# Optimization experiments

Measured on AMD Instinct MI355X. Metric: run time of the kernel, lower is better.

The kernel has to match this reference:

```python
import jax, jax.numpy as jnp
import numpy as np

N_NODES = 100000
N_EDGES = 1600000
D = 128


def setup_inputs() -> dict:
    key = jax.random.key(0)
    k1, k2, k3, k4 = jax.random.split(key, 4)
    ego_embeddings = jax.random.normal(k1, (N_NODES, D), dtype=jnp.float32)
    edge_index = jax.random.randint(k2, (2, N_EDGES), 0, N_NODES, dtype=jnp.int64)
    edge_weight = jax.random.uniform(k3, (N_EDGES,), dtype=jnp.float32)
    W = jax.random.normal(k4, (D, D), dtype=jnp.float32) * (1.0 / np.sqrt(D))
    b = jnp.zeros((D,), dtype=jnp.float32)
    return {"ego_embeddings": ego_embeddings, "edge_index": edge_index,
            "edge_weight": edge_weight, "W": W, "b": b}


def reference(ego_embeddings, edge_index, edge_weight, W, b):
    # SpMM: side[i] = sum_j A[i,j] * ego[j], A given as COO (dst=row, src=col)
    src = edge_index[1]
    dst = edge_index[0]
    messages = ego_embeddings[src] * edge_weight[:, None]  # [E, D]
    side_embeddings = jax.ops.segment_sum(messages, dst, num_segments=N_NODES)
    # gcn aggregator: LeakyReLU(Linear(ego + side)); dropout p=0.0 -> identity
    h = (ego_embeddings + side_embeddings) @ W.T + b
    return jax.nn.leaky_relu(h, negative_slope=0.01)
```

## Files before the change

### kernel.cpp

```cpp
#include <hip/hip_runtime.h>

#define N_NODES 100000
#define N_EDGES 1600000
#define DIM 128
#define CAP 48

#define NBIN 1563
#define BINW 64
#define BCAP 1280
#define EPT  8
#define EPB  2048

#define WB_OFF   0
#define GCUR_OFF 32768
#define DEG_OFF  65536
#define EPK_OFF  465536
#define EGOB_OFF (EPK_OFF + (size_t)N_NODES * CAP * 4)
#define WS_BF16  (EGOB_OFF + (size_t)N_NODES * DIM * 2)

using short8  = __attribute__((ext_vector_type(8))) short;
using floatx4 = __attribute__((ext_vector_type(4))) float;

static __device__ __forceinline__ unsigned short f2bf(float f) {
    unsigned u = __float_as_uint(f);
    u += 0x7FFF + ((u >> 16) & 1);
    return (unsigned short)(u >> 16);
}
static __device__ __forceinline__ float bf_lo(unsigned u) {
    return __uint_as_float(u << 16);
}
static __device__ __forceinline__ float bf_hi(unsigned u) {
    return __uint_as_float(u & 0xFFFF0000u);
}

#define EGO_BLKS 6250
__global__ __launch_bounds__(256) void convert_all(
        const float4* __restrict__ e4, uint4* __restrict__ o4,
        const float* __restrict__ W, unsigned short* __restrict__ Wb,
        int* __restrict__ gcur) {
    const int b = blockIdx.x;
    const int tid = threadIdx.x;
    if (b < EGO_BLKS) {
        int i = b * 256 + tid;
        float4 a = e4[2 * i];
        float4 c = e4[2 * i + 1];
        uint4 o;
        o.x = (unsigned)f2bf(a.x) | ((unsigned)f2bf(a.y) << 16);
        o.y = (unsigned)f2bf(a.z) | ((unsigned)f2bf(a.w) << 16);
        o.z = (unsigned)f2bf(c.x) | ((unsigned)f2bf(c.y) << 16);
        o.w = (unsigned)f2bf(c.z) | ((unsigned)f2bf(c.w) << 16);
        o4[i] = o;
    } else {
        int j = (b - EGO_BLKS) * 256 + tid;
        if (j < DIM * DIM) Wb[j] = f2bf(W[j]);
        if (j < NBIN) gcur[j] = 0;
    }
}

__global__ __launch_bounds__(256) void convert_w(const float* __restrict__ W,
                                                 unsigned short* __restrict__ Wb) {
    int i = blockIdx.x * 256 + threadIdx.x;
    if (i < DIM * DIM) Wb[i] = f2bf(W[i]);
}

__global__ __launch_bounds__(256) void bin_edges(
        const int* __restrict__ eidx,
        const float* __restrict__ ew,
        int* __restrict__ gcur,
        uint2* __restrict__ stg) {
    __shared__ int lh[NBIN];
    __shared__ int gb[NBIN];
    const int tid = threadIdx.x;
    const int b0 = blockIdx.x * EPB;

    for (int i = tid; i < NBIN; i += 256) lh[i] = 0;
    __syncthreads();

    int dst[EPT], rank[EPT];
    unsigned rec[EPT];
    bool val[EPT];
#pragma unroll
    for (int k = 0; k < EPT; ++k) {
        int e = b0 + k * 256 + tid;
        val[k] = e < N_EDGES;
        int ec = val[k] ? e : 0;
        int d = eidx[ec];
        int s = eidx[N_EDGES + ec];
        float w = ew[ec];
        dst[k] = d;
        rec[k] = ((unsigned)s << 15) | (unsigned)(w * 32767.0f + 0.5f);
        rank[k] = val[k] ? atomicAdd(&lh[d >> 6], 1) : 0;
    }
    __syncthreads();

    for (int i = tid; i < NBIN; i += 256) {
        int c = lh[i];
        gb[i] = c ? atomicAdd(&gcur[i], c) : 0;
    }
    __syncthreads();

#pragma unroll
    for (int k = 0; k < EPT; ++k) {
        if (val[k]) {
            int bin = dst[k] >> 6;
            int pos = gb[bin] + rank[k];
            if (pos < BCAP)
                stg[(size_t)bin * BCAP + pos] = make_uint2(rec[k], (unsigned)dst[k]);
        }
    }
}

__global__ __launch_bounds__(256) void place_edges(
        const uint2* __restrict__ stg,
        const int* __restrict__ gcur,
        unsigned* __restrict__ epk,
        int* __restrict__ deg) {
    __shared__ int lc[BINW];
    const int tid = threadIdx.x;
    const int bin = blockIdx.x;

    if (tid < BINW) lc[tid] = 0;
    __syncthreads();

    int cnt = gcur[bin];
    if (cnt > BCAP) cnt = BCAP;
    for (int r = tid; r < cnt; r += 256) {
        uint2 rc = stg[(size_t)bin * BCAP + r];
        int d = (int)rc.y;
        int rk = atomicAdd(&lc[d & (BINW - 1)], 1);
        if (rk < CAP) epk[(size_t)d * CAP + rk] = rc.x;
    }
    __syncthreads();

    if (tid < BINW) {
        int node = bin * BINW + tid;
        if (node < N_NODES) deg[node] = lc[tid];
    }
}

__global__ __launch_bounds__(256) void csr_scatter(
        const int* __restrict__ eidx,
        const float* __restrict__ ew,
        int* __restrict__ deg,
        unsigned* __restrict__ epk) {
    int e = blockIdx.x * 256 + threadIdx.x;
    if (e >= N_EDGES) return;
    int dst = eidx[e];
    int src = eidx[N_EDGES + e];
    float w = ew[e];
    int r = atomicAdd(&deg[dst], 1);
    if (r < CAP) {
        unsigned q = (unsigned)(w * 32767.0f + 0.5f);
        epk[(size_t)dst * CAP + r] = ((unsigned)src << 15) | q;
    }
}

#define LSTR 136
template <bool BF16>
__global__ __launch_bounds__(256, 6) void gather_gemm(
        const unsigned* __restrict__ eg2,
        const float* __restrict__ egof,
        const unsigned* __restrict__ epk,
        const int* __restrict__ deg,
        const unsigned short* __restrict__ Wb,
        const float* __restrict__ bias,
        float* __restrict__ out) {
    __shared__ __align__(16) unsigned short s_x[64 * LSTR];

    const int tid  = threadIdx.x;
    const int wave = tid >> 6;
    const int lane = tid & 63;
    const int R    = blockIdx.x * 64;
    const float inv15 = 1.0f / 32767.0f;

    if (BF16) {
        const int half = lane >> 5;
        const int hl   = lane & 31;
        const uint2* eg8 = (const uint2*)eg2;
        const int plane = (lane < CAP) ? lane : (CAP - 1);

        int nA = R + wave * 16;
        int nB = nA + 1;
        unsigned pvA = (nA < N_NODES) ? epk[(size_t)nA * CAP + plane] : 0u;
        unsigned pvB = (nB < N_NODES) ? epk[(size_t)nB * CAP + plane] : 0u;
        int dgA = (nA < N_NODES) ? deg[nA] : 0;
        int dgB = (nB < N_NODES) ? deg[nB] : 0;

        for (int i = 0; i < 8; ++i) {
            const int myNode = R + wave * 16 + 2 * i + half;
            const bool valid = myNode < N_NODES;

            unsigned pvAc = pvA, pvBc = pvB;
            int dgAc = dgA < CAP ? dgA : CAP;
            int dgBc = dgB < CAP ? dgB : CAP;
            const int dgme = half ? dgBc : dgAc;
            const int dgw  = dgAc > dgBc ? dgAc : dgBc;

            if (i < 7) {
                int mA = R + wave * 16 + 2 * (i + 1);
                int mB = mA + 1;
                pvA = (mA < N_NODES) ? epk[(size_t)mA * CAP + plane] : 0u;
                pvB = (mB < N_NODES) ? epk[(size_t)mB * CAP + plane] : 0u;
                dgA = (mA < N_NODES) ? deg[mA] : 0;
                dgB = (mB < N_NODES) ? deg[mB] : 0;
            }

            uint2 idv = make_uint2(0u, 0u);
            if (valid) idv = eg8[(size_t)myNode * 32 + hl];

            float acc[4][4];
#pragma unroll
            for (int k = 0; k < 4; ++k)
#pragma unroll
                for (int c = 0; c < 4; ++c) acc[k][c] = 0.f;
            acc[0][0] = bf_lo(idv.x);  acc[0][1] = bf_hi(idv.x);
            acc[0][2] = bf_lo(idv.y);  acc[0][3] = bf_hi(idv.y);

            for (int e = 0; e < dgw; e += 8) {
                unsigned p[8];
                uint2 g[8];
#pragma unroll
                for (int k = 0; k < 8; ++k) {
                    unsigned pa = __shfl(pvAc, e + k);
                    unsigned pb = __shfl(pvBc, e + k);
                    unsigned ps = half ? pb : pa;
                    p[k] = ((e + k) < dgme) ? ps : 0u;
                }
#pragma unroll
                for (int k = 0; k < 8; ++k)
                    g[k] = eg8[(size_t)(p[k] >> 15) * 32 + hl];
#pragma unroll
                for (int k = 0; k < 8; ++k) {
                    float wv = (float)(p[k] & 0x7FFF) * inv15;
                    acc[k & 3][0] = fmaf(wv, bf_lo(g[k].x), acc[k & 3][0]);
                    acc[k & 3][1] = fmaf(wv, bf_hi(g[k].x), acc[k & 3][1]);
                    acc[k & 3][2] = fmaf(wv, bf_lo(g[k].y), acc[k & 3][2]);
                    acc[k & 3][3] = fmaf(wv, bf_hi(g[k].y), acc[k & 3][3]);
                }
            }

            float s0 = (acc[0][0] + acc[1][0]) + (acc[2][0] + acc[3][0]);
            float s1 = (acc[0][1] + acc[1][1]) + (acc[2][1] + acc[3][1]);
            float s2 = (acc[0][2] + acc[1][2]) + (acc[2][2] + acc[3][2]);
            float s3 = (acc[0][3] + acc[1][3]) + (acc[2][3] + acc[3][3]);

            unsigned lo = (unsigned)f2bf(s0) | ((unsigned)f2bf(s1) << 16);
            unsigned hi = (unsigned)f2bf(s2) | ((unsigned)f2bf(s3) << 16);
            int myRow = wave * 16 + 2 * i + half;
            *(uint2*)&s_x[myRow * LSTR + hl * 4] = make_uint2(lo, hi);
        }
    } else {
        for (int i = 0; i < 16; ++i) {
            int node = R + wave * 16 + i;
            float ax = 0.f, ay = 0.f, bx = 0.f, by = 0.f;
            float cx = 0.f, cy = 0.f, dx2 = 0.f, dy2 = 0.f;
            if (node < N_NODES) {
                size_t cidx = (size_t)node * 64 + lane;
                float2 vv = ((const float2*)egof)[cidx];
                ax = vv.x; ay = vv.y;
                int dg = deg[node];
                if (dg > CAP) dg = CAP;
                size_t base = (size_t)node * CAP;
                unsigned pv = epk[base + (lane < CAP ? lane : CAP - 1)];
                int e = 0;
                for (; e + 3 < dg; e += 4) {
                    unsigned p0 = __shfl(pv, e + 0);
                    unsigned p1 = __shfl(pv, e + 1);
                    unsigned p2 = __shfl(pv, e + 2);
                    unsigned p3 = __shfl(pv, e + 3);
                    float2 v0 = ((const float2*)egof)[(size_t)(p0 >> 15) * 64 + lane];
                    float2 v1 = ((const float2*)egof)[(size_t)(p1 >> 15) * 64 + lane];
                    float2 v2 = ((const float2*)egof)[(size_t)(p2 >> 15) * 64 + lane];
                    float2 v3 = ((const float2*)egof)[(size_t)(p3 >> 15) * 64 + lane];
                    float w0 = (float)(p0 & 0x7FFF) * inv15;
                    float w1 = (float)(p1 & 0x7FFF) * inv15;
                    float w2 = (float)(p2 & 0x7FFF) * inv15;
                    float w3 = (float)(p3 & 0x7FFF) * inv15;
                    ax = fmaf(w0, v0.x, ax);  ay = fmaf(w0, v0.y, ay);
                    bx = fmaf(w1, v1.x, bx);  by = fmaf(w1, v1.y, by);
                    cx = fmaf(w2, v2.x, cx);  cy = fmaf(w2, v2.y, cy);
                    dx2 = fmaf(w3, v3.x, dx2); dy2 = fmaf(w3, v3.y, dy2);
                }
                for (; e < dg; ++e) {
                    unsigned p = __shfl(pv, e);
                    float2 vv2 = ((const float2*)egof)[(size_t)(p >> 15) * 64 + lane];
                    float w = (float)(p & 0x7FFF) * inv15;
                    ax = fmaf(w, vv2.x, ax);  ay = fmaf(w, vv2.y, ay);
                }
            }
            unsigned pk = (unsigned)f2bf(ax + bx + cx + dx2) |
                          ((unsigned)f2bf(ay + by + cy + dy2) << 16);
            *(unsigned*)&s_x[(wave * 16 + i) * LSTR + 2 * lane] = pk;
        }
    }

    const int m0 = wave * 16;
    const int ml = lane & 15;
    const int q  = lane >> 4;

    floatx4 acc[8];
#pragma unroll
    for (int nt = 0; nt < 8; ++nt) acc[nt] = (floatx4){0.f, 0.f, 0.f, 0.f};

#pragma unroll
    for (int kc = 0; kc < 4; ++kc) {
        short8 a = *(const short8*)&s_x[(m0 + ml) * LSTR + kc * 32 + q * 8];
#pragma unroll
        for (int nt = 0; nt < 8; ++nt) {
            short8 b = *(const short8*)&Wb[(size_t)(nt * 16 + ml) * DIM + kc * 32 + q * 8];
            acc[nt] = __builtin_amdgcn_mfma_f32_16x16x32_bf16(a, b, acc[nt], 0, 0, 0);
        }
    }

#pragma unroll
    for (int nt = 0; nt < 8; ++nt) {
        int col = nt * 16 + ml;
        float bv = bias[col];
#pragma unroll
        for (int r = 0; r < 4; ++r) {
            int row = R + m0 + q * 4 + r;
            if (row < N_NODES) {
                float v = acc[nt][r] + bv;
                v = v > 0.f ? v : 0.01f * v;
                out[(size_t)row * DIM + col] = v;
            }
        }
    }
}

extern "C" void kernel_launch(void* const* d_in, const int* in_sizes, int n_in,
                              void* d_out, int out_size, void* d_ws, size_t ws_size,
                              hipStream_t stream) {
    const float* ego  = (const float*)d_in[0];
    const int*   eidx = (const int*)d_in[1];
    const float* ew   = (const float*)d_in[2];
    const float* W    = (const float*)d_in[3];
    const float* bias = (const float*)d_in[4];
    float* out = (float*)d_out;

    char* ws = (char*)d_ws;
    unsigned short* Wb   = (unsigned short*)(ws + WB_OFF);
    int*            gcur = (int*)(ws + GCUR_OFF);
    int*            deg  = (int*)(ws + DEG_OFF);
    unsigned*       epk  = (unsigned*)(ws + EPK_OFF);
    unsigned short* egob = (unsigned short*)(ws + EGOB_OFF);
    uint2*          stg  = (uint2*)out;

    const bool use_bf16 = (ws_size >= WS_BF16);

    if (use_bf16) {
        convert_all<<<EGO_BLKS + 64, 256, 0, stream>>>(
            (const float4*)ego, (uint4*)egob, W, Wb, gcur);
        bin_edges<<<(N_EDGES + EPB - 1) / EPB, 256, 0, stream>>>(
            eidx, ew, gcur, stg);
        place_edges<<<NBIN, 256, 0, stream>>>(stg, gcur, epk, deg);
        gather_gemm<true><<<(N_NODES + 63) / 64, 256, 0, stream>>>(
            (const unsigned*)egob, ego, epk, deg, Wb, bias, out);
    } else {
        convert_w<<<(DIM * DIM + 255) / 256, 256, 0, stream>>>(W, Wb);
        hipMemsetAsync(deg, 0, (size_t)N_NODES * sizeof(int), stream);
        csr_scatter<<<(N_EDGES + 255) / 256, 256, 0, stream>>>(
            eidx, ew, deg, epk);
        gather_gemm<false><<<(N_NODES + 63) / 64, 256, 0, stream>>>(
            (const unsigned*)egob, ego, epk, deg, Wb, bias, out);
    }
}
```

Baseline: 265.8 us.

## Replace binned edge placement with direct atomic scatter and shrink gather blocks

Drops the two-pass bin_edges/place_edges build of the padded per-node edge lists. It goes back to a single csr_scatter kernel that does a global atomicAdd per edge on the degree array, which convert_all now zeroes. The gather_gemm kernel moves from 64-row, 256-thread blocks to 32-row, 128-thread blocks, doubling the block count for better occupancy and tail balance. The risk is that contended global atomics and scattered epk writes cost more than the binned path they replace, and smaller blocks reuse each W tile across fewer rows.

Result: slower. 314.1 us (+18.1%).

```diff
diff --git a/kernel.cpp b/kernel.cpp
--- a/kernel.cpp
+++ b/kernel.cpp
@@ -5,14 +5,7 @@
 #define DIM 128
 #define CAP 48
 
-#define NBIN 1563
-#define BINW 64
-#define BCAP 1280
-#define EPT  8
-#define EPB  2048
-
 #define WB_OFF   0
-#define GCUR_OFF 32768
 #define DEG_OFF  65536
 #define EPK_OFF  465536
 #define EGOB_OFF (EPK_OFF + (size_t)N_NODES * CAP * 4)
@@ -34,10 +27,11 @@
 }
 
 #define EGO_BLKS 6250
+#define TAIL_BLKS 391
 __global__ __launch_bounds__(256) void convert_all(
         const float4* __restrict__ e4, uint4* __restrict__ o4,
         const float* __restrict__ W, unsigned short* __restrict__ Wb,
-        int* __restrict__ gcur) {
+        int* __restrict__ deg) {
     const int b = blockIdx.x;
     const int tid = threadIdx.x;
     if (b < EGO_BLKS) {
@@ -53,7 +47,7 @@
     } else {
         int j = (b - EGO_BLKS) * 256 + tid;
         if (j < DIM * DIM) Wb[j] = f2bf(W[j]);
-        if (j < NBIN) gcur[j] = 0;
+        if (j < N_NODES) deg[j] = 0;
     }
 }
 
@@ -61,81 +55,6 @@
                                                  unsigned short* __restrict__ Wb) {
     int i = blockIdx.x * 256 + threadIdx.x;
     if (i < DIM * DIM) Wb[i] = f2bf(W[i]);
-}
-
-__global__ __launch_bounds__(256) void bin_edges(
-        const int* __restrict__ eidx,
-        const float* __restrict__ ew,
-        int* __restrict__ gcur,
-        uint2* __restrict__ stg) {
-    __shared__ int lh[NBIN];
-    __shared__ int gb[NBIN];
-    const int tid = threadIdx.x;
-    const int b0 = blockIdx.x * EPB;
-
-    for (int i = tid; i < NBIN; i += 256) lh[i] = 0;
-    __syncthreads();
-
-    int dst[EPT], rank[EPT];
-    unsigned rec[EPT];
-    bool val[EPT];
-#pragma unroll
-    for (int k = 0; k < EPT; ++k) {
-        int e = b0 + k * 256 + tid;
-        val[k] = e < N_EDGES;
-        int ec = val[k] ? e : 0;
-        int d = eidx[ec];
-        int s = eidx[N_EDGES + ec];
-        float w = ew[ec];
-        dst[k] = d;
-        rec[k] = ((unsigned)s << 15) | (unsigned)(w * 32767.0f + 0.5f);
-        rank[k] = val[k] ? atomicAdd(&lh[d >> 6], 1) : 0;
-    }
-    __syncthreads();
-
-    for (int i = tid; i < NBIN; i += 256) {
-        int c = lh[i];
-        gb[i] = c ? atomicAdd(&gcur[i], c) : 0;
-    }
-    __syncthreads();
-
-#pragma unroll
-    for (int k = 0; k < EPT; ++k) {
-        if (val[k]) {
-            int bin = dst[k] >> 6;
-            int pos = gb[bin] + rank[k];
-            if (pos < BCAP)
-                stg[(size_t)bin * BCAP + pos] = make_uint2(rec[k], (unsigned)dst[k]);
-        }
-    }
-}
-
-__global__ __launch_bounds__(256) void place_edges(
-        const uint2* __restrict__ stg,
-        const int* __restrict__ gcur,
-        unsigned* __restrict__ epk,
-        int* __restrict__ deg) {
-    __shared__ int lc[BINW];
-    const int tid = threadIdx.x;
-    const int bin = blockIdx.x;
-
-    if (tid < BINW) lc[tid] = 0;
-    __syncthreads();
-
-    int cnt = gcur[bin];
-    if (cnt > BCAP) cnt = BCAP;
-    for (int r = tid; r < cnt; r += 256) {
-        uint2 rc = stg[(size_t)bin * BCAP + r];
-        int d = (int)rc.y;
-        int rk = atomicAdd(&lc[d & (BINW - 1)], 1);
-        if (rk < CAP) epk[(size_t)d * CAP + rk] = rc.x;
-    }
-    __syncthreads();
-
-    if (tid < BINW) {
-        int node = bin * BINW + tid;
-        if (node < N_NODES) deg[node] = lc[tid];
-    }
 }
 
 __global__ __launch_bounds__(256) void csr_scatter(
@@ -155,9 +74,10 @@
     }
 }
 
+#define ROWS 32
 #define LSTR 136
 template <bool BF16>
-__global__ __launch_bounds__(256, 6) void gather_gemm(
+__global__ __launch_bounds__(128, 8) void gather_gemm(
         const unsigned* __restrict__ eg2,
         const float* __restrict__ egof,
         const unsigned* __restrict__ epk,
@@ -165,12 +85,12 @@
         const unsigned short* __restrict__ Wb,
         const float* __restrict__ bias,
         float* __restrict__ out) {
-    __shared__ __align__(16) unsigned short s_x[64 * LSTR];
+    __shared__ __align__(16) unsigned short s_x[ROWS * LSTR];
 
     const int tid  = threadIdx.x;
     const int wave = tid >> 6;
     const int lane = tid & 63;
-    const int R    = blockIdx.x * 64;
+    const int R    = blockIdx.x * ROWS;
     const float inv15 = 1.0f / 32767.0f;
 
     if (BF16) {
@@ -340,28 +260,25 @@
 
     char* ws = (char*)d_ws;
     unsigned short* Wb   = (unsigned short*)(ws + WB_OFF);
-    int*            gcur = (int*)(ws + GCUR_OFF);
     int*            deg  = (int*)(ws + DEG_OFF);
     unsigned*       epk  = (unsigned*)(ws + EPK_OFF);
     unsigned short* egob = (unsigned short*)(ws + EGOB_OFF);
-    uint2*          stg  = (uint2*)out;
 
     const bool use_bf16 = (ws_size >= WS_BF16);
 
     if (use_bf16) {
-        convert_all<<<EGO_BLKS + 64, 256, 0, stream>>>(
-            (const float4*)ego, (uint4*)egob, W, Wb, gcur);
-        bin_edges<<<(N_EDGES + EPB - 1) / EPB, 256, 0, stream>>>(
-            eidx, ew, gcur, stg);
-        place_edges<<<NBIN, 256, 0, stream>>>(stg, gcur, epk, deg);
-        gather_gemm<true><<<(N_NODES + 63) / 64, 256, 0, stream>>>(
+        convert_all<<<EGO_BLKS + TAIL_BLKS, 256, 0, stream>>>(
+            (const float4*)ego, (uint4*)egob, W, Wb, deg);
+        csr_scatter<<<(N_EDGES + 255) / 256, 256, 0, stream>>>(
+            eidx, ew, deg, epk);
+        gather_gemm<true><<<(N_NODES + ROWS - 1) / ROWS, 128, 0, stream>>>(
             (const unsigned*)egob, ego, epk, deg, Wb, bias, out);
     } else {
         convert_w<<<(DIM * DIM + 255) / 256, 256, 0, stream>>>(W, Wb);
         hipMemsetAsync(deg, 0, (size_t)N_NODES * sizeof(int), stream);
         csr_scatter<<<(N_EDGES + 255) / 256, 256, 0, stream>>>(
             eidx, ew, deg, epk);
-        gather_gemm<false><<<(N_NODES + 63) / 64, 256, 0, stream>>>(
+        gather_gemm<false><<<(N_NODES + ROWS - 1) / ROWS, 128, 0, stream>>>(
             (const unsigned*)egob, ego, epk, deg, Wb, bias, out);
     }
 }
```

## Fuse edge placement into gather-GEMM via per-bin shared-memory CSR build

Applied to the files above, without the earlier changes.

Removes the separate place_edges pass and its global epk/deg arrays: each gather-GEMM block now reads its bin's staged records and builds the per-node edge lists in shared memory before gathering. Binning now uses a two-pass scheme (count, then re-read and place) over larger 8192-edge blocks instead of keeping records in registers. The staging buffer moves from the output buffer to the workspace. This saves one kernel launch and a global write/read of the edge lists, at the cost of more LDS per block (occupancy hint lowered to 5) and a second read of the edge inputs during binning.

Result: no change. 270.9 us (+1.9%).

```diff
diff --git a/kernel.cpp b/kernel.cpp
--- a/kernel.cpp
+++ b/kernel.cpp
@@ -8,15 +8,17 @@
 #define NBIN 1563
 #define BINW 64
 #define BCAP 1280
-#define EPT  8
-#define EPB  2048
+#define EPB  8192
+#define NBBLK ((N_EDGES + EPB - 1) / EPB)
 
 #define WB_OFF   0
 #define GCUR_OFF 32768
+#define STG_OFF  65536
+#define EGOB_OFF (STG_OFF + (size_t)NBIN * BCAP * 8)
+#define WS_BF16  (EGOB_OFF + (size_t)N_NODES * DIM * 2)
+
 #define DEG_OFF  65536
 #define EPK_OFF  465536
-#define EGOB_OFF (EPK_OFF + (size_t)N_NODES * CAP * 4)
-#define WS_BF16  (EGOB_OFF + (size_t)N_NODES * DIM * 2)
 
 using short8  = __attribute__((ext_vector_type(8))) short;
 using floatx4 = __attribute__((ext_vector_type(4))) float;
@@ -34,6 +36,7 @@
 }
 
 #define EGO_BLKS 6250
+#define TAIL_BLKS 64
 __global__ __launch_bounds__(256) void convert_all(
         const float4* __restrict__ e4, uint4* __restrict__ o4,
         const float* __restrict__ W, unsigned short* __restrict__ Wb,
@@ -63,7 +66,7 @@
     if (i < DIM * DIM) Wb[i] = f2bf(W[i]);
 }
 
-__global__ __launch_bounds__(256) void bin_edges(
+__global__ __launch_bounds__(256) void bin2scan(
         const int* __restrict__ eidx,
         const float* __restrict__ ew,
         int* __restrict__ gcur,
@@ -76,65 +79,174 @@
     for (int i = tid; i < NBIN; i += 256) lh[i] = 0;
     __syncthreads();
 
-    int dst[EPT], rank[EPT];
-    unsigned rec[EPT];
-    bool val[EPT];
-#pragma unroll
-    for (int k = 0; k < EPT; ++k) {
+    for (int k = 0; k < EPB / 256; ++k) {
         int e = b0 + k * 256 + tid;
-        val[k] = e < N_EDGES;
-        int ec = val[k] ? e : 0;
-        int d = eidx[ec];
-        int s = eidx[N_EDGES + ec];
-        float w = ew[ec];
-        dst[k] = d;
-        rec[k] = ((unsigned)s << 15) | (unsigned)(w * 32767.0f + 0.5f);
-        rank[k] = val[k] ? atomicAdd(&lh[d >> 6], 1) : 0;
+        if (e < N_EDGES) atomicAdd(&lh[eidx[e] >> 6], 1);
     }
     __syncthreads();
 
     for (int i = tid; i < NBIN; i += 256) {
         int c = lh[i];
         gb[i] = c ? atomicAdd(&gcur[i], c) : 0;
-    }
-    __syncthreads();
-
-#pragma unroll
-    for (int k = 0; k < EPT; ++k) {
-        if (val[k]) {
-            int bin = dst[k] >> 6;
-            int pos = gb[bin] + rank[k];
+        lh[i] = 0;
+    }
+    __syncthreads();
+
+    for (int k = 0; k < EPB / 256; ++k) {
+        int e = b0 + k * 256 + tid;
+        if (e < N_EDGES) {
+            int d = eidx[e];
+            int s = eidx[N_EDGES + e];
+            float w = ew[e];
+            unsigned rec = ((unsigned)s << 15) | (unsigned)(w * 32767.0f + 0.5f);
+            int bin = d >> 6;
+            int pos = gb[bin] + atomicAdd(&lh[bin], 1);
             if (pos < BCAP)
-                stg[(size_t)bin * BCAP + pos] = make_uint2(rec[k], (unsigned)dst[k]);
-        }
-    }
-}
-
-__global__ __launch_bounds__(256) void place_edges(
+                stg[(size_t)bin * BCAP + pos] = make_uint2(rec, (unsigned)d);
+        }
+    }
+}
+
+#define LSTR 136
+__global__ __launch_bounds__(256, 5) void bin_gather_gemm(
+        const unsigned* __restrict__ eg2,
         const uint2* __restrict__ stg,
         const int* __restrict__ gcur,
-        unsigned* __restrict__ epk,
-        int* __restrict__ deg) {
-    __shared__ int lc[BINW];
-    const int tid = threadIdx.x;
-    const int bin = blockIdx.x;
-
-    if (tid < BINW) lc[tid] = 0;
+        const unsigned short* __restrict__ Wb,
+        const float* __restrict__ bias,
+        float* __restrict__ out) {
+    __shared__ __align__(16) unsigned short s_x[BINW * LSTR];
+    __shared__ unsigned s_epk[BINW * CAP];
+    __shared__ int s_lc[BINW];
+
+    const int tid  = threadIdx.x;
+    const int wave = tid >> 6;
+    const int lane = tid & 63;
+    const int bin  = blockIdx.x;
+    const int R    = bin * BINW;
+    const float inv15 = 1.0f / 32767.0f;
+    const uint2* eg8 = (const uint2*)eg2;
+
+    if (tid < BINW) s_lc[tid] = 0;
     __syncthreads();
 
     int cnt = gcur[bin];
     if (cnt > BCAP) cnt = BCAP;
+    const uint2* bstg = stg + (size_t)bin * BCAP;
     for (int r = tid; r < cnt; r += 256) {
-        uint2 rc = stg[(size_t)bin * BCAP + r];
-        int d = (int)rc.y;
-        int rk = atomicAdd(&lc[d & (BINW - 1)], 1);
-        if (rk < CAP) epk[(size_t)d * CAP + rk] = rc.x;
-    }
-    __syncthreads();
-
-    if (tid < BINW) {
-        int node = bin * BINW + tid;
-        if (node < N_NODES) deg[node] = lc[tid];
+        uint2 rc = bstg[r];
+        int d6 = (int)(rc.y & (BINW - 1));
+        int rk = atomicAdd(&s_lc[d6], 1);
+        if (rk < CAP) s_epk[d6 * CAP + rk] = rc.x;
+    }
+    __syncthreads();
+
+    {
+        const int half = lane >> 5;
+        const int hl   = lane & 31;
+        const int plane = (lane < CAP) ? lane : (CAP - 1);
+
+        int lA = wave * 16;
+        unsigned pvA = s_epk[lA * CAP + plane];
+        unsigned pvB = s_epk[(lA + 1) * CAP + plane];
+        int dgA = s_lc[lA];
+        int dgB = s_lc[lA + 1];
+
+        for (int i = 0; i < 8; ++i) {
+            const int myNode = R + wave * 16 + 2 * i + half;
+            const bool valid = myNode < N_NODES;
+
+            unsigned pvAc = pvA, pvBc = pvB;
+            int dgAc = dgA < CAP ? dgA : CAP;
+            int dgBc = dgB < CAP ? dgB : CAP;
+            const int dgme = half ? dgBc : dgAc;
+            const int dgw  = dgAc > dgBc ? dgAc : dgBc;
+
+            if (i < 7) {
+                int mA = wave * 16 + 2 * (i + 1);
+                pvA = s_epk[mA * CAP + plane];
+                pvB = s_epk[(mA + 1) * CAP + plane];
+                dgA = s_lc[mA];
+                dgB = s_lc[mA + 1];
+            }
+
+            uint2 idv = make_uint2(0u, 0u);
+            if (valid) idv = eg8[(size_t)myNode * 32 + hl];
+
+            float acc[4][4];
+#pragma unroll
+            for (int k = 0; k < 4; ++k)
+#pragma unroll
+                for (int c = 0; c < 4; ++c) acc[k][c] = 0.f;
+            acc[0][0] = bf_lo(idv.x);  acc[0][1] = bf_hi(idv.x);
+            acc[0][2] = bf_lo(idv.y);  acc[0][3] = bf_hi(idv.y);
+
+            for (int e = 0; e < dgw; e += 8) {
+                unsigned p[8];
+                uint2 g[8];
+#pragma unroll
+                for (int k = 0; k < 8; ++k) {
+                    unsigned pa = __shfl(pvAc, e + k);
+                    unsigned pb = __shfl(pvBc, e + k);
+                    unsigned ps = half ? pb : pa;
+                    p[k] = ((e + k) < dgme) ? ps : 0u;
+                }
+#pragma unroll
+                for (int k = 0; k < 8; ++k)
+                    g[k] = eg8[(size_t)(p[k] >> 15) * 32 + hl];
+#pragma unroll
+                for (int k = 0; k < 8; ++k) {
+                    float wv = (float)(p[k] & 0x7FFF) * inv15;
+                    acc[k & 3][0] = fmaf(wv, bf_lo(g[k].x), acc[k & 3][0]);
+                    acc[k & 3][1] = fmaf(wv, bf_hi(g[k].x), acc[k & 3][1]);
+                    acc[k & 3][2] = fmaf(wv, bf_lo(g[k].y), acc[k & 3][2]);
+                    acc[k & 3][3] = fmaf(wv, bf_hi(g[k].y), acc[k & 3][3]);
+                }
+            }
+
+            float s0 = (acc[0][0] + acc[1][0]) + (acc[2][0] + acc[3][0]);
+            float s1 = (acc[0][1] + acc[1][1]) + (acc[2][1] + acc[3][1]);
+            float s2 = (acc[0][2] + acc[1][2]) + (acc[2][2] + acc[3][2]);
+            float s3 = (acc[0][3] + acc[1][3]) + (acc[2][3] + acc[3][3]);
+
+            unsigned lo = (unsigned)f2bf(s0) | ((unsigned)f2bf(s1) << 16);
+            unsigned hi = (unsigned)f2bf(s2) | ((unsigned)f2bf(s3) << 16);
+            int myRow = wave * 16 + 2 * i + half;
+            *(uint2*)&s_x[myRow * LSTR + hl * 4] = make_uint2(lo, hi);
+        }
+    }
+
+    const int m0 = wave * 16;
+    const int ml = lane & 15;
+    const int q  = lane >> 4;
+
+    floatx4 acc[8];
+#pragma unroll
+    for (int nt = 0; nt < 8; ++nt) acc[nt] = (floatx4){0.f, 0.f, 0.f, 0.f};
+
+#pragma unroll
+    for (int kc = 0; kc < 4; ++kc) {
+        short8 a = *(const short8*)&s_x[(m0 + ml) * LSTR + kc * 32 + q * 8];
+#pragma unroll
+        for (int nt = 0; nt < 8; ++nt) {
+            short8 b = *(const short8*)&Wb[(size_t)(nt * 16 + ml) * DIM + kc * 32 + q * 8];
+            acc[nt] = __builtin_amdgcn_mfma_f32_16x16x32_bf16(a, b, acc[nt], 0, 0, 0);
+        }
+    }
+
+#pragma unroll
+    for (int nt = 0; nt < 8; ++nt) {
+        int col = nt * 16 + ml;
+        float bv = bias[col];
+#pragma unroll
+        for (int r = 0; r < 4; ++r) {
+            int row = R + m0 + q * 4 + r;
+            if (row < N_NODES) {
+                float v = acc[nt][r] + bv;
+                v = v > 0.f ? v : 0.01f * v;
+                out[(size_t)row * DIM + col] = v;
+            }
+        }
     }
 }
 
@@ -155,10 +267,7 @@
     }
 }
 
-#define LSTR 136
-template <bool BF16>
-__global__ __launch_bounds__(256, 6) void gather_gemm(
-        const unsigned* __restrict__ eg2,
+__global__ __launch_bounds__(256) void gather_gemm_f32(
         const float* __restrict__ egof,
         const unsigned* __restrict__ epk,
         const int* __restrict__ deg,
@@ -173,125 +282,47 @@
     const int R    = blockIdx.x * 64;
     const float inv15 = 1.0f / 32767.0f;
 
-    if (BF16) {
-        const int half = lane >> 5;
-        const int hl   = lane & 31;
-        const uint2* eg8 = (const uint2*)eg2;
-        const int plane = (lane < CAP) ? lane : (CAP - 1);
-
-        int nA = R + wave * 16;
-        int nB = nA + 1;
-        unsigned pvA = (nA < N_NODES) ? epk[(size_t)nA * CAP + plane] : 0u;
-        unsigned pvB = (nB < N_NODES) ? epk[(size_t)nB * CAP + plane] : 0u;
-        int dgA = (nA < N_NODES) ? deg[nA] : 0;
-        int dgB = (nB < N_NODES) ? deg[nB] : 0;
-
-        for (int i = 0; i < 8; ++i) {
-            const int myNode = R + wave * 16 + 2 * i + half;
-            const bool valid = myNode < N_NODES;
-
-            unsigned pvAc = pvA, pvBc = pvB;
-            int dgAc = dgA < CAP ? dgA : CAP;
-            int dgBc = dgB < CAP ? dgB : CAP;
-            const int dgme = half ? dgBc : dgAc;
-            const int dgw  = dgAc > dgBc ? dgAc : dgBc;
-
-            if (i < 7) {
-                int mA = R + wave * 16 + 2 * (i + 1);
-                int mB = mA + 1;
-                pvA = (mA < N_NODES) ? epk[(size_t)mA * CAP + plane] : 0u;
-                pvB = (mB < N_NODES) ? epk[(size_t)mB * CAP + plane] : 0u;
-                dgA = (mA < N_NODES) ? deg[mA] : 0;
-                dgB = (mB < N_NODES) ? deg[mB] : 0;
-            }
-
-            uint2 idv = make_uint2(0u, 0u);
-            if (valid) idv = eg8[(size_t)myNode * 32 + hl];
-
-            float acc[4][4];
-#pragma unroll
-            for (int k = 0; k < 4; ++k)
-#pragma unroll
-                for (int c = 0; c < 4; ++c) acc[k][c] = 0.f;
-            acc[0][0] = bf_lo(idv.x);  acc[0][1] = bf_hi(idv.x);
-            acc[0][2] = bf_lo(idv.y);  acc[0][3] = bf_hi(idv.y);
-
-            for (int e = 0; e < dgw; e += 8) {
-                unsigned p[8];
-                uint2 g[8];
-#pragma unroll
-                for (int k = 0; k < 8; ++k) {
-                    unsigned pa = __shfl(pvAc, e + k);
-                    unsigned pb = __shfl(pvBc, e + k);
-                    unsigned ps = half ? pb : pa;
-                    p[k] = ((e + k) < dgme) ? ps : 0u;
-                }
-#pragma unroll
-                for (int k = 0; k < 8; ++k)
-                    g[k] = eg8[(size_t)(p[k] >> 15) * 32 + hl];
-#pragma unroll
-                for (int k = 0; k < 8; ++k) {
-                    float wv = (float)(p[k] & 0x7FFF) * inv15;
-                    acc[k & 3][0] = fmaf(wv, bf_lo(g[k].x), acc[k & 3][0]);
-                    acc[k & 3][1] = fmaf(wv, bf_hi(g[k].x), acc[k & 3][1]);
-                    acc[k & 3][2] = fmaf(wv, bf_lo(g[k].y), acc[k & 3][2]);
-                    acc[k & 3][3] = fmaf(wv, bf_hi(g[k].y), acc[k & 3][3]);
-                }
-            }
-
-            float s0 = (acc[0][0] + acc[1][0]) + (acc[2][0] + acc[3][0]);
-            float s1 = (acc[0][1] + acc[1][1]) + (acc[2][1] + acc[3][1]);
-            float s2 = (acc[0][2] + acc[1][2]) + (acc[2][2] + acc[3][2]);
-            float s3 = (acc[0][3] + acc[1][3]) + (acc[2][3] + acc[3][3]);
-
-            unsigned lo = (unsigned)f2bf(s0) | ((unsigned)f2bf(s1) << 16);
-            unsigned hi = (unsigned)f2bf(s2) | ((unsigned)f2bf(s3) << 16);
-            int myRow = wave * 16 + 2 * i + half;
-            *(uint2*)&s_x[myRow * LSTR + hl * 4] = make_uint2(lo, hi);
-        }
-    } else {
-        for (int i = 0; i < 16; ++i) {
-            int node = R + wave * 16 + i;
-            float ax = 0.f, ay = 0.f, bx = 0.f, by = 0.f;
-            float cx = 0.f, cy = 0.f, dx2 = 0.f, dy2 = 0.f;
-            if (node < N_NODES) {
-                size_t cidx = (size_t)node * 64 + lane;
-                float2 vv = ((const float2*)egof)[cidx];
-                ax = vv.x; ay = vv.y;
-                int dg = deg[node];
-                if (dg > CAP) dg = CAP;
-                size_t base = (size_t)node * CAP;
-                unsigned pv = epk[base + (lane < CAP ? lane : CAP - 1)];
-                int e = 0;
-                for (; e + 3 < dg; e += 4) {
-                    unsigned p0 = __shfl(pv, e + 0);
-                    unsigned p1 = __shfl(pv, e + 1);
-                    unsigned p2 = __shfl(pv, e + 2);
-                    unsigned p3 = __shfl(pv, e + 3);
-                    float2 v0 = ((const float2*)egof)[(size_t)(p0 >> 15) * 64 + lane];
-                    float2 v1 = ((const float2*)egof)[(size_t)(p1 >> 15) * 64 + lane];
-                    float2 v2 = ((const float2*)egof)[(size_t)(p2 >> 15) * 64 + lane];
-                    float2 v3 = ((const float2*)egof)[(size_t)(p3 >> 15) * 64 + lane];
-                    float w0 = (float)(p0 & 0x7FFF) * inv15;
-                    float w1 = (float)(p1 & 0x7FFF) * inv15;
-                    float w2 = (float)(p2 & 0x7FFF) * inv15;
-                    float w3 = (float)(p3 & 0x7FFF) * inv15;
-                    ax = fmaf(w0, v0.x, ax);  ay = fmaf(w0, v0.y, ay);
-                    bx = fmaf(w1, v1.x, bx);  by = fmaf(w1, v1.y, by);
-                    cx = fmaf(w2, v2.x, cx);  cy = fmaf(w2, v2.y, cy);
-                    dx2 = fmaf(w3, v3.x, dx2); dy2 = fmaf(w3, v3.y, dy2);
-                }
-                for (; e < dg; ++e) {
-                    unsigned p = __shfl(pv, e);
-                    float2 vv2 = ((const float2*)egof)[(size_t)(p >> 15) * 64 + lane];
-                    float w = (float)(p & 0x7FFF) * inv15;
-                    ax = fmaf(w, vv2.x, ax);  ay = fmaf(w, vv2.y, ay);
-                }
-            }
-            unsigned pk = (unsigned)f2bf(ax + bx + cx + dx2) |
-                          ((unsigned)f2bf(ay + by + cy + dy2) << 16);
-            *(unsigned*)&s_x[(wave * 16 + i) * LSTR + 2 * lane] = pk;
-        }
+    for (int i = 0; i < 16; ++i) {
+        int node = R + wave * 16 + i;
+        float ax = 0.f, ay = 0.f, bx = 0.f, by = 0.f;
+        float cx = 0.f, cy = 0.f, dx2 = 0.f, dy2 = 0.f;
+        if (node < N_NODES) {
+            size_t cidx = (size_t)node * 64 + lane;
+            float2 vv = ((const float2*)egof)[cidx];
+            ax = vv.x; ay = vv.y;
+            int dg = deg[node];
+            if (dg > CAP) dg = CAP;
+            size_t base = (size_t)node * CAP;
+            unsigned pv = epk[base + (lane < CAP ? lane : CAP - 1)];
+            int e = 0;
+            for (; e + 3 < dg; e += 4) {
+                unsigned p0 = __shfl(pv, e + 0);
+                unsigned p1 = __shfl(pv, e + 1);
+                unsigned p2 = __shfl(pv, e + 2);
+                unsigned p3 = __shfl(pv, e + 3);
+                float2 v0 = ((const float2*)egof)[(size_t)(p0 >> 15) * 64 + lane];
+                float2 v1 = ((const float2*)egof)[(size_t)(p1 >> 15) * 64 + lane];
+                float2 v2 = ((const float2*)egof)[(size_t)(p2 >> 15) * 64 + lane];
+                float2 v3 = ((const float2*)egof)[(size_t)(p3 >> 15) * 64 + lane];
+                float w0 = (float)(p0 & 0x7FFF) * inv15;
+                float w1 = (float)(p1 & 0x7FFF) * inv15;
+                float w2 = (float)(p2 & 0x7FFF) * inv15;
+                float w3 = (float)(p3 & 0x7FFF) * inv15;
+                ax = fmaf(w0, v0.x, ax);  ay = fmaf(w0, v0.y, ay);
+                bx = fmaf(w1, v1.x, bx);  by = fmaf(w1, v1.y, by);
+                cx = fmaf(w2, v2.x, cx);  cy = fmaf(w2, v2.y, cy);
+                dx2 = fmaf(w3, v3.x, dx2); dy2 = fmaf(w3, v3.y, dy2);
+            }
+            for (; e < dg; ++e) {
+                unsigned p = __shfl(pv, e);
+                float2 vv2 = ((const float2*)egof)[(size_t)(p >> 15) * 64 + lane];
+                float w = (float)(p & 0x7FFF) * inv15;
+                ax = fmaf(w, vv2.x, ax);  ay = fmaf(w, vv2.y, ay);
+            }
+        }
+        unsigned pk = (unsigned)f2bf(ax + bx + cx + dx2) |
+                      ((unsigned)f2bf(ay + by + cy + dy2) << 16);
+        *(unsigned*)&s_x[(wave * 16 + i) * LSTR + 2 * lane] = pk;
     }
 
     const int m0 = wave * 16;
@@ -341,27 +372,25 @@
     char* ws = (char*)d_ws;
     unsigned short* Wb   = (unsigned short*)(ws + WB_OFF);
     int*            gcur = (int*)(ws + GCUR_OFF);
-    int*            deg  = (int*)(ws + DEG_OFF);
-    unsigned*       epk  = (unsigned*)(ws + EPK_OFF);
+    uint2*          stg  = (uint2*)(ws + STG_OFF);
     unsigned short* egob = (unsigned short*)(ws + EGOB_OFF);
-    uint2*          stg  = (uint2*)out;
 
     const bool use_bf16 = (ws_size >= WS_BF16);
 
     if (use_bf16) {
-        convert_all<<<EGO_BLKS + 64, 256, 0, stream>>>(
+        convert_all<<<EGO_BLKS + TAIL_BLKS, 256, 0, stream>>>(
             (const float4*)ego, (uint4*)egob, W, Wb, gcur);
-        bin_edges<<<(N_EDGES + EPB - 1) / EPB, 256, 0, stream>>>(
-            eidx, ew, gcur, stg);
-        place_edges<<<NBIN, 256, 0, stream>>>(stg, gcur, epk, deg);
-        gather_gemm<true><<<(N_NODES + 63) / 64, 256, 0, stream>>>(
-            (const unsigned*)egob, ego, epk, deg, Wb, bias, out);
+        bin2scan<<<NBBLK, 256, 0, stream>>>(eidx, ew, gcur, stg);
+        bin_gather_gemm<<<NBIN, 256, 0, stream>>>(
+            (const unsigned*)egob, stg, gcur, Wb, bias, out);
     } else {
+        int*      deg = (int*)(ws + DEG_OFF);
+        unsigned* epk = (unsigned*)(ws + EPK_OFF);
         convert_w<<<(DIM * DIM + 255) / 256, 256, 0, stream>>>(W, Wb);
         hipMemsetAsync(deg, 0, (size_t)N_NODES * sizeof(int), stream);
         csr_scatter<<<(N_EDGES + 255) / 256, 256, 0, stream>>>(
             eidx, ew, deg, epk);
-        gather_gemm<false><<<(N_NODES + 63) / 64, 256, 0, stream>>>(
-            (const unsigned*)egob, ego, epk, deg, Wb, bias, out);
-    }
-}
+        gather_gemm_f32<<<(N_NODES + 63) / 64, 256, 0, stream>>>(
+            ego, epk, deg, Wb, bias, out);
+    }
+}
```
